# Performance work log

Measured on AMD Instinct MI355X. Metric: run time of the kernel, lower is better.

Reference implementation:

```python
import jax, jax.numpy as jnp
import numpy as np

N_AUTHOR, N_PAPER = 20000, 40000
E = 400000
IN_DIM, HIDDEN, HEADS, NUM_CLASSES, NUM_LAYERS = 128, 128, 8, 16, 2
DIM = HIDDEN // HEADS
NEG_SLOPE = 0.2
AUTHOR_RAW = 64


def setup_inputs() -> dict:
    key = jax.random.key(0)
    ks = jax.random.split(key, 16)
    s = 0.05
    return {
        'x_author': jax.random.normal(ks[0], (N_AUTHOR, AUTHOR_RAW), jnp.float32),
        'x_paper': jax.random.normal(ks[1], (N_PAPER, IN_DIM), jnp.float32),
        'Wa': jax.random.normal(ks[2], (AUTHOR_RAW, IN_DIM), jnp.float32) * s,
        'proj_w': jax.random.normal(ks[3], (NUM_LAYERS, 2, IN_DIM, HIDDEN), jnp.float32) * s,
        'proj_b': jnp.zeros((NUM_LAYERS, 2, HIDDEN), jnp.float32),
        'att_src': jax.random.normal(ks[4], (NUM_LAYERS, 3, HEADS, DIM), jnp.float32) * s,
        'att_dst': jax.random.normal(ks[5], (NUM_LAYERS, 3, HEADS, DIM), jnp.float32) * s,
        'klin_w': jax.random.normal(ks[6], (NUM_LAYERS, HIDDEN, HIDDEN), jnp.float32) * s,
        'klin_b': jnp.zeros((NUM_LAYERS, HIDDEN), jnp.float32),
        'q': jax.random.normal(ks[7], (NUM_LAYERS, HIDDEN), jnp.float32) * s,
        'lin_w': jax.random.normal(ks[8], (HIDDEN, NUM_CLASSES), jnp.float32) * s,
        'lin_b': jnp.zeros((NUM_CLASSES,), jnp.float32),
        'ei_writes': jnp.stack([jax.random.randint(ks[9], (E,), 0, N_AUTHOR),
                                jax.random.randint(ks[10], (E,), 0, N_PAPER)]),
        'ei_written_by': jnp.stack([jax.random.randint(ks[11], (E,), 0, N_PAPER),
                                    jax.random.randint(ks[12], (E,), 0, N_AUTHOR)]),
        'ei_cites': jnp.stack([jax.random.randint(ks[13], (E,), 0, N_PAPER),
                               jax.random.randint(ks[14], (E,), 0, N_PAPER)]),
    }


def _segment_softmax(scores, seg, num_segments):
    # scores: [E, H]; softmax over edges sharing a destination node.
    m = jax.ops.segment_max(scores, seg, num_segments=num_segments)
    m = jnp.where(jnp.isfinite(m), m, 0.0)
    e = jnp.exp(scores - m[seg])
    denom = jax.ops.segment_sum(e, seg, num_segments=num_segments)
    return e / (denom[seg] + 1e-16)


def _han_forward(x_author, x_paper, Wa, proj_w, proj_b, att_src, att_dst,
                 klin_w, klin_b, q, lin_w, lin_b,
                 ei_writes, ei_written_by, ei_cites):
    # Type-alignment projector (author: 64 -> 128, no bias; paper: Identity)
    x = {'author': x_author @ Wa, 'paper': x_paper}
    nsize = {'author': N_AUTHOR, 'paper': N_PAPER}
    ntidx = {'author': 0, 'paper': 1}
    edge_types = [('author', 'paper', ei_writes),
                  ('paper', 'author', ei_written_by),
                  ('paper', 'paper', ei_cites)]
    for l in range(NUM_LAYERS):
        # Per-node-type projection -> [N, H, D]
        xh = {nt: (x[nt] @ proj_w[l, ntidx[nt]] + proj_b[l, ntidx[nt]]).reshape(-1, HEADS, DIM)
              for nt in x}
        outs = {'author': [], 'paper': []}
        for e_id, (src, dst, ei) in enumerate(edge_types):
            a_src = (xh[src] * att_src[l, e_id]).sum(-1)  # [N_src, H]
            a_dst = (xh[dst] * att_dst[l, e_id]).sum(-1)  # [N_dst, H]
            si, di = ei[0], ei[1]
            alpha = a_src[si] + a_dst[di]                 # [E, H]
            alpha = jnp.where(alpha >= 0, alpha, NEG_SLOPE * alpha)  # leaky_relu
            alpha = _segment_softmax(alpha, di, nsize[dst])
            # attention dropout omitted (eval mode)
            msg = (xh[src][si] * alpha[:, :, None]).reshape(-1, HIDDEN)  # [E, HIDDEN]
            agg = jax.ops.segment_sum(msg, di, num_segments=nsize[dst])
            outs[dst].append(jax.nn.relu(agg))
        # Semantic-level attention over metapath embeddings per node type
        newx = {}
        for nt, xs in outs.items():
            stk = jnp.stack(xs)  # [M, N, F]
            score = (q[l] * jnp.tanh(stk @ klin_w[l] + klin_b[l]).mean(axis=1)).sum(-1)  # [M]
            attn = jax.nn.softmax(score)
            newx[nt] = (attn[:, None, None] * stk).sum(0)
        x = newx
        if l < NUM_LAYERS - 1:
            x = {nt: jax.nn.relu(v) for nt, v in x.items()}
            # feature dropout omitted (eval mode)
    return x['paper'] @ lin_w + lin_b  # [N_PAPER, NUM_CLASSES]


def reference(x_author, x_paper, Wa, proj_w, proj_b, att_src, att_dst,
              klin_w, klin_b, q, lin_w, lin_b,
              ei_writes, ei_written_by, ei_cites):
    return _han_forward(x_author, x_paper, Wa, proj_w, proj_b, att_src, att_dst,
                        klin_w, klin_b, q, lin_w, lin_b,
                        ei_writes, ei_written_by, ei_cites)
```

## Files before the change

### kernel.cpp

```cpp
#include <hip/hip_runtime.h>
#include <hip/hip_bf16.h>

typedef __hip_bfloat16 bf16;
typedef __hip_bfloat162 bf162;

#define N_AUTHOR 20000
#define N_PAPER  40000
#define NEDGE    400000
#define HID      128
#define HEADS    8
#define DIMH     16
#define NCLS     16

typedef short short4v __attribute__((ext_vector_type(4)));
typedef short short8v __attribute__((ext_vector_type(8)));
typedef float f32x4   __attribute__((ext_vector_type(4)));

__device__ __forceinline__ bf162 mk2(float a, float b){
    bf162 r; r.x = __float2bfloat16(a); r.y = __float2bfloat16(b); return r;
}
__device__ __forceinline__ float b2f(short s){
    return __uint_as_float(((unsigned)(unsigned short)s) << 16);
}
__device__ __forceinline__ short f2bs(float v){
    unsigned u = __float_as_uint(v);
    unsigned r = (u + 0x7FFFu + ((u >> 16) & 1u)) >> 16;
    return (short)r;
}
__device__ __forceinline__ float fastrcp(float x){ return __builtin_amdgcn_rcpf(x); }

__device__ __forceinline__ float fast_tanh(float x){
    x = fminf(fmaxf(x, -15.f), 15.f);
    float e = __expf(2.f * x);
    return 1.f - 2.f * fastrcp(e + 1.f);
}

template<int KDIM, int EPI>
__device__ __forceinline__ void bgemm_body(
    const bf16* __restrict__ A, const bf16* __restrict__ Wt, const float* __restrict__ Bb,
    bf16* __restrict__ C, const float* __restrict__ qv, float* __restrict__ score,
    int M, int brow, float* red)
{
    const int tid  = threadIdx.x;
    const int lane = tid & 63;
    const int wv   = tid >> 6;
    const int lr   = lane & 15;
    const int quad = lane >> 4;
    const int row0 = brow * 64 + wv * 16;
    const int arow_i = row0 + lr;
    const bool rowok = arow_i < M;
    const bf16* arow = A + (long)arow_i * KDIM;

    short8v afrag[KDIM / 32];
    #pragma unroll
    for (int kc = 0; kc < KDIM / 32; kc++) {
        short8v f = {0,0,0,0,0,0,0,0};
        if (rowok) f = *(const short8v*)(arow + kc * 32 + quad * 8);
        afrag[kc] = f;
    }

    f32x4 acc[8];
    #pragma unroll
    for (int ct = 0; ct < 8; ct++) acc[ct] = (f32x4){0.f, 0.f, 0.f, 0.f};

    #pragma unroll
    for (int k0 = 0; k0 < KDIM / 32; k0 += 2) {
        short8v bf[2][8];
        #pragma unroll
        for (int u = 0; u < 2; u++)
            #pragma unroll
            for (int ct = 0; ct < 8; ct++)
                bf[u][ct] = *(const short8v*)(Wt + (long)(ct * 16 + lr) * KDIM + (k0 + u) * 32 + quad * 8);
        #pragma unroll
        for (int u = 0; u < 2; u++)
            #pragma unroll
            for (int ct = 0; ct < 8; ct++)
                acc[ct] = __builtin_amdgcn_mfma_f32_16x16x32_bf16(afrag[k0 + u], bf[u][ct], acc[ct], 0, 0, 0);
    }

    if (EPI == 0) {
        #pragma unroll
        for (int ct = 0; ct < 8; ct++) {
            float bc = Bb ? Bb[ct * 16 + lr] : 0.f;
            #pragma unroll
            for (int r = 0; r < 4; r++) {
                int orow = row0 + quad * 4 + r;
                if (orow < M)
                    C[(long)orow * HID + ct * 16 + lr] = __float2bfloat16(acc[ct][r] + bc);
            }
        }
    } else {
        float part = 0.f;
        #pragma unroll
        for (int ct = 0; ct < 8; ct++) {
            float bc = Bb ? Bb[ct * 16 + lr] : 0.f;
            float qc = qv[ct * 16 + lr];
            #pragma unroll
            for (int r = 0; r < 4; r++) {
                int orow = row0 + quad * 4 + r;
                if (orow < M) part += qc * fast_tanh(acc[ct][r] + bc);
            }
        }
        red[tid] = part;
        __syncthreads();
        for (int s = 128; s > 0; s >>= 1) {
            if (tid < s) red[tid] += red[tid + s];
            __syncthreads();
        }
        if (tid == 0) atomicAdd(score, red[0]);
    }
}

template<int KDIM, int EPI>
__global__ __launch_bounds__(256) void bgemm_pair_kernel(
    const bf16* __restrict__ A0, const bf16* __restrict__ Wt0, const float* __restrict__ Bb0,
    bf16* __restrict__ C0, float* __restrict__ score0, int M0, int NB0,
    const bf16* __restrict__ A1, const bf16* __restrict__ Wt1, const float* __restrict__ Bb1,
    bf16* __restrict__ C1, float* __restrict__ score1, int M1,
    const float* __restrict__ qv)
{
    __shared__ float red[256];
    const int bx = blockIdx.x;
    if (bx < NB0)
        bgemm_body<KDIM, EPI>(A0, Wt0, Bb0, C0, qv, score0, M0, bx, red);
    else
        bgemm_body<KDIM, EPI>(A1, Wt1, Bb1, C1, qv, score1, M1, bx - NB0, red);
}

#define R_WA  (128 * 64)
#define R_PW  (4 * 128 * 128)
#define R_KW  (2 * 128 * 128)
#define NXA (N_AUTHOR * 64)
#define NXP (N_PAPER * HID)
#define CONV_W_TOT (R_WA + R_PW + R_KW)
#define CONV_X_TOT ((NXA + NXP) / 4)
#define CONV_TOT   (CONV_W_TOT + CONV_X_TOT)

#define CNT_OFF1 N_PAPER
#define CNT_OFF2 (N_PAPER + N_AUTHOR)
#define NDEST    (2 * N_PAPER + N_AUTHOR)
#define NCOPY 8
#define CW    2
#define CIDX(c, d) (((c) * NDEST + (d)) * CW)
#define CNT_TOT (NCOPY * NDEST * CW)
#define E3 (3 * NEDGE)
#define HIST_T (E3 / 4)

__global__ __launch_bounds__(256) void conv_hist_kernel(
    const int* __restrict__ d0, const int* __restrict__ d1, const int* __restrict__ d2,
    int* __restrict__ cnt, unsigned short* __restrict__ rank, int HB,
    const float* __restrict__ Wa, const float* __restrict__ proj_w,
    const float* __restrict__ klin_w,
    const float* __restrict__ xa_f, const float* __restrict__ xp_f,
    bf16* __restrict__ wt_wa, bf16* __restrict__ wt_proj, bf16* __restrict__ wt_klin,
    bf16* __restrict__ xa, bf16* __restrict__ xp)
{
    int bx = blockIdx.x;
    if (bx < HB) {
        int c = bx & (NCOPY - 1);
        int* mycnt = cnt + c * NDEST * CW;
        int t = bx * 256 + threadIdx.x;
        if (t >= HIST_T) return;
        #pragma unroll
        for (int u = 0; u < 4; u++) {
            int i = t + u * HIST_T;
            int r;
            if (i < NEDGE)            r = atomicAdd(&mycnt[d0[i] * CW], 1);
            else if (i < 2*NEDGE)     r = atomicAdd(&mycnt[(CNT_OFF1 + d1[i - NEDGE]) * CW], 1);
            else                      r = atomicAdd(&mycnt[(CNT_OFF2 + d2[i - 2*NEDGE]) * CW], 1);
            rank[i] = (unsigned short)((c << 13) | r);
        }
        return;
    }
    int t = (bx - HB) * 256 + threadIdx.x;
    if (t < CONV_W_TOT) {
        int i = t;
        if (i < R_WA) {
            int n = i >> 6, k = i & 63;
            wt_wa[i] = __float2bfloat16(Wa[k * 128 + n]);
        } else if (i < R_WA + R_PW) {
            int j = i - R_WA;
            int m = j >> 14, r = j & 16383;
            int n = r >> 7, k = r & 127;
            wt_proj[j] = __float2bfloat16(proj_w[m * 16384 + k * 128 + n]);
        } else {
            int j = i - R_WA - R_PW;
            int m = j >> 14, r = j & 16383;
            int n = r >> 7, k = r & 127;
            wt_klin[j] = __float2bfloat16(klin_w[m * 16384 + k * 128 + n]);
        }
    } else if (t < CONV_TOT) {
        int i = (t - CONV_W_TOT) * 4;
        if (i < NXA) {
            float4 v = *(const float4*)(xa_f + i);
            xa[i]   = __float2bfloat16(v.x); xa[i+1] = __float2bfloat16(v.y);
            xa[i+2] = __float2bfloat16(v.z); xa[i+3] = __float2bfloat16(v.w);
        } else {
            int j = i - NXA;
            float4 v = *(const float4*)(xp_f + j);
            xp[j]   = __float2bfloat16(v.x); xp[j+1] = __float2bfloat16(v.y);
            xp[j+2] = __float2bfloat16(v.z); xp[j+3] = __float2bfloat16(v.w);
        }
    }
}

__device__ __forceinline__ int job_nd(int j){ return j == 1 ? N_AUTHOR : N_PAPER; }
__device__ __forceinline__ int job_off(int j){ return j == 0 ? 0 : (j == 1 ? CNT_OFF1 : CNT_OFF2); }

__global__ __launch_bounds__(256) void scan_a3_kernel(const int* __restrict__ cnt,
                                                      int* __restrict__ bsum)
{
    int j = blockIdx.y;
    int nd = job_nd(j), off = job_off(j);
    __shared__ int s[256];
    int tid = threadIdx.x;
    int i = blockIdx.x * 256 + tid;
    int v = 0;
    if (i < nd) {
        #pragma unroll
        for (int c = 0; c < NCOPY; c++) v += cnt[CIDX(c, off + i)];
    }
    s[tid] = v;
    __syncthreads();
    for (int st = 128; st > 0; st >>= 1) {
        if (tid < st) s[tid] += s[tid + st];
        __syncthreads();
    }
    if (tid == 0) bsum[j * 256 + blockIdx.x] = s[0];
}

__global__ __launch_bounds__(256) void scan_b3_kernel(int* __restrict__ bsum,
    int* __restrict__ roff0, int* __restrict__ roff1, int* __restrict__ roff2)
{
    int j = blockIdx.x;
    int nd = job_nd(j);
    int nb = (nd + 255) / 256;
    int* roff = j == 0 ? roff0 : (j == 1 ? roff1 : roff2);
    __shared__ int s[256];
    int tid = threadIdx.x;
    int v = (tid < nb) ? bsum[j * 256 + tid] : 0;
    s[tid] = v;
    __syncthreads();
    for (int off = 1; off < 256; off <<= 1) {
        int t = (tid >= off) ? s[tid - off] : 0;
        __syncthreads();
        s[tid] += t;
        __syncthreads();
    }
    if (tid < nb) bsum[j * 256 + tid] = s[tid] - v;
    if (tid == 255) roff[nd] = s[255];
}

__global__ __launch_bounds__(256) void scan_c3_kernel(int* __restrict__ cnt,
    const int* __restrict__ bsum,
    int* __restrict__ roff0, int* __restrict__ roff1, int* __restrict__ roff2)
{
    int j = blockIdx.y;
    int nd = job_nd(j), off = job_off(j);
    int* roff = j == 0 ? roff0 : (j == 1 ? roff1 : roff2);
    __shared__ int s[256];
    int tid = threadIdx.x;
    int i = blockIdx.x * 256 + tid;
    int cc[NCOPY];
    int v = 0;
    if (i < nd) {
        #pragma unroll
        for (int c = 0; c < NCOPY; c++) { cc[c] = cnt[CIDX(c, off + i)]; v += cc[c]; }
    }
    s[tid] = v;
    __syncthreads();
    for (int o = 1; o < 256; o <<= 1) {
        int t = (tid >= o) ? s[tid - o] : 0;
        __syncthreads();
        s[tid] += t;
        __syncthreads();
    }
    if (i < nd) {
        int base = bsum[j * 256 + blockIdx.x] + s[tid] - v;
        roff[i] = base;
        #pragma unroll
        for (int c = 0; c < NCOPY; c++) { cnt[CIDX(c, off + i)] = base; base += cc[c]; }
    }
}

__global__ __launch_bounds__(256) void fill_gemm_kernel(
    const bf16* __restrict__ A, const bf16* __restrict__ Wt, bf16* __restrict__ C,
    int M, int GAb,
    const int* __restrict__ s0, const int* __restrict__ d0,
    const int* __restrict__ s1, const int* __restrict__ d1,
    const int* __restrict__ s2, const int* __restrict__ d2,
    const int* __restrict__ cnt,
    const unsigned short* __restrict__ rank,
    unsigned short* __restrict__ c0, unsigned short* __restrict__ c1, unsigned short* __restrict__ c2)
{
    __shared__ float red[256];
    int bx = blockIdx.x;
    if (bx < GAb) {
        bgemm_body<64, 0>(A, Wt, nullptr, C, nullptr, nullptr, M, bx, red);
        return;
    }
    int t = (bx - GAb) * 256 + threadIdx.x;
    if (t >= HIST_T) return;
    #pragma unroll
    for (int u = 0; u < 4; u++) {
        int i = t + u * HIST_T;
        int rw = rank[i];
        int c = rw >> 13, rk = rw & 0x1FFF;
        if (i < NEDGE) {
            int d = d0[i];
            c0[cnt[CIDX(c, d)] + rk] = (unsigned short)s0[i];
        } else if (i < 2*NEDGE) {
            int e = i - NEDGE, d = d1[e];
            c1[cnt[CIDX(c, CNT_OFF1 + d)] + rk] = (unsigned short)s1[e];
        } else {
            int e = i - 2*NEDGE, d = d2[e];
            c2[cnt[CIDX(c, CNT_OFF2 + d)] + rk] = (unsigned short)s2[e];
        }
    }
}

__global__ void node_att_multi_kernel(const bf16* __restrict__ xh,
    const float* __restrict__ A0, const float* __restrict__ A1,
    const float* __restrict__ A2, const float* __restrict__ A3,
    float* __restrict__ O0, float* __restrict__ O1,
    float* __restrict__ O2, float* __restrict__ O3, int N)
{
    int i = blockIdx.x * blockDim.x + threadIdx.x;
    if (i >= N * HEADS) return;
    int n = i >> 3, h = i & 7;
    const bf16* row = xh + (long)n * HID + h * DIMH;
    float x[DIMH];
    #pragma unroll
    for (int d = 0; d < DIMH; d++) x[d] = __bfloat162float(row[d]);
    if (A0) { float s = 0.f;
        #pragma unroll
        for (int d = 0; d < DIMH; d++) s += x[d] * A0[h*DIMH + d];
        O0[i] = s; }
    if (A1) { float s = 0.f;
        #pragma unroll
        for (int d = 0; d < DIMH; d++) s += x[d] * A1[h*DIMH + d];
        O1[i] = s; }
    if (A2) { float s = 0.f;
        #pragma unroll
        for (int d = 0; d < DIMH; d++) s += x[d] * A2[h*DIMH + d];
        O2[i] = s; }
    if (A3) { float s = 0.f;
        #pragma unroll
        for (int d = 0; d < DIMH; d++) s += x[d] * A3[h*DIMH + d];
        O3[i] = s; }
}

__global__ __launch_bounds__(256) void paper_gather2_kernel(
    const int* __restrict__ roff0, const unsigned short* __restrict__ csrc0,
    const float* __restrict__ as0, const float* __restrict__ ad0,
    const bf16* __restrict__ xha,
    const int* __restrict__ roff2, const unsigned short* __restrict__ csrc2,
    const float* __restrict__ as2, const float* __restrict__ ad2,
    const bf16* __restrict__ xhp,
    bf16* __restrict__ out0, bf16* __restrict__ out2)
{
    int lane = threadIdx.x & 63;
    int li   = lane & 15;
    int sub  = lane >> 4;
    int w = blockIdx.x * 16 + (threadIdx.x >> 6) * 4 + sub;
    if (w >= N_PAPER) return;
    int h = li >> 1;

    int b0 = roff0[w], n0 = roff0[w + 1] - b0;
    int b2 = roff2[w], n2 = roff2[w + 1] - b2;
    float ad0v = ad0[(long)w * 8 + h];
    float ad2v = ad2[(long)w * 8 + h];
    float den0 = 0.f, den2 = 0.f;
    float acc0[8], acc2[8];
    #pragma unroll
    for (int j = 0; j < 8; j++) { acc0[j] = 0.f; acc2[j] = 0.f; }

    int nmax = n0 > n2 ? n0 : n2;
    int c0m = n0 > 0 ? n0 - 1 : 0;
    int c2m = n2 > 0 ? n2 - 1 : 0;
    for (int i = 0; i < nmax; i += 4) {
        int sA[4], sB[4];
        #pragma unroll
        for (int u = 0; u < 4; u++) {
            sA[u] = csrc0[b0 + min(i + u, c0m)];
            sB[u] = csrc2[b2 + min(i + u, c2m)];
        }
        float aA[4], aB[4];
        short8v xA[4], xB[4];
        #pragma unroll
        for (int u = 0; u < 4; u++) {
            aA[u] = as0[(long)sA[u] * 8 + h];
            xA[u] = *(const short8v*)(xha + (long)sA[u] * HID + li * 8);
            aB[u] = as2[(long)sB[u] * 8 + h];
            xB[u] = *(const short8v*)(xhp + (long)sB[u] * HID + li * 8);
        }
        #pragma unroll
        for (int u = 0; u < 4; u++) {
            float a = aA[u] + ad0v;
            a = a >= 0.f ? a : 0.2f * a;
            float wt = __expf(fminf(a, 60.f));
            wt = (i + u < n0) ? wt : 0.f;
            den0 += wt;
            #pragma unroll
            for (int j = 0; j < 8; j++)
                acc0[j] = fmaf(b2f(xA[u][j]), wt, acc0[j]);
            a = aB[u] + ad2v;
            a = a >= 0.f ? a : 0.2f * a;
            wt = __expf(fminf(a, 60.f));
            wt = (i + u < n2) ? wt : 0.f;
            den2 += wt;
            #pragma unroll
            for (int j = 0; j < 8; j++)
                acc2[j] = fmaf(b2f(xB[u][j]), wt, acc2[j]);
        }
    }
    float inv0 = fastrcp(den0 + 1e-16f);
    float inv2 = fastrcp(den2 + 1e-16f);
    short8v o0, o2;
    #pragma unroll
    for (int j = 0; j < 8; j++) {
        o0[j] = f2bs(fmaxf(acc0[j] * inv0, 0.f));
        o2[j] = f2bs(fmaxf(acc2[j] * inv2, 0.f));
    }
    *(short8v*)(out0 + (long)w * HID + li * 8) = o0;
    *(short8v*)(out2 + (long)w * HID + li * 8) = o2;
}

__global__ __launch_bounds__(256) void edge_gather_kernel(
    const int* __restrict__ roff, const unsigned short* __restrict__ csrc,
    const float* __restrict__ as_, const float* __restrict__ ad_,
    const bf16* __restrict__ xh, bf16* __restrict__ out, int Ndst)
{
    int lane = threadIdx.x & 63;
    int li   = lane & 15;
    int sub  = lane >> 4;
    int w = blockIdx.x * 16 + (threadIdx.x >> 6) * 4 + sub;
    if (w >= Ndst) return;
    int h = li >> 1;
    int beg = roff[w], n = roff[w + 1] - beg;
    float adv = ad_[(long)w * 8 + h];
    float den = 0.f;
    float acc[8];
    #pragma unroll
    for (int j = 0; j < 8; j++) acc[j] = 0.f;
    int cm = n > 0 ? n - 1 : 0;
    for (int i = 0; i < n; i += 4) {
        int s[4];
        #pragma unroll
        for (int u = 0; u < 4; u++) s[u] = csrc[beg + min(i + u, cm)];
        float av[4]; short8v xv[4];
        #pragma unroll
        for (int u = 0; u < 4; u++) {
            av[u] = as_[(long)s[u] * 8 + h];
            xv[u] = *(const short8v*)(xh + (long)s[u] * HID + li * 8);
        }
        #pragma unroll
        for (int u = 0; u < 4; u++) {
            float a = av[u] + adv;
            a = a >= 0.f ? a : 0.2f * a;
            float wt = __expf(fminf(a, 60.f));
            wt = (i + u < n) ? wt : 0.f;
            den += wt;
            #pragma unroll
            for (int j = 0; j < 8; j++)
                acc[j] = fmaf(b2f(xv[u][j]), wt, acc[j]);
        }
    }
    float inv = fastrcp(den + 1e-16f);
    short8v o;
    #pragma unroll
    for (int j = 0; j < 8; j++) o[j] = f2bs(fmaxf(acc[j] * inv, 0.f));
    *(short8v*)(out + (long)w * HID + li * 8) = o;
}

__global__ void combine_kernel(const bf16* __restrict__ a0, const bf16* __restrict__ a1,
                               const float* __restrict__ score, bf16* __restrict__ out, int n2)
{
    int i = blockIdx.x * blockDim.x + threadIdx.x;
    if (i >= n2) return;
    float s0 = score[0] * (1.f / N_PAPER);
    float s1 = score[1] * (1.f / N_PAPER);
    float m = fmaxf(s0, s1);
    float e0 = __expf(s0 - m), e1 = __expf(s1 - m);
    float inv = fastrcp(e0 + e1);
    float w0 = e0 * inv, w1 = e1 * inv;
    bf162 v0 = ((const bf162*)a0)[i];
    bf162 v1 = ((const bf162*)a1)[i];
    ((bf162*)out)[i] = mk2(w0 * __bfloat162float(v0.x) + w1 * __bfloat162float(v1.x),
                           w0 * __bfloat162float(v0.y) + w1 * __bfloat162float(v1.y));
}

__global__ __launch_bounds__(256) void final_lin_fused_kernel(
    const bf16* __restrict__ a0, const bf16* __restrict__ a1,
    const float* __restrict__ score,
    const float* __restrict__ W, const float* __restrict__ B, float* __restrict__ out)
{
    __shared__ float Ws[HID * NCLS];
    int tid = threadIdx.x;
    for (int i = tid; i < HID * NCLS; i += 256) Ws[i] = W[i];
    __syncthreads();
    float s0 = score[0] * (1.f / N_PAPER);
    float s1 = score[1] * (1.f / N_PAPER);
    float m = fmaxf(s0, s1);
    float e0 = __expf(s0 - m), e1 = __expf(s1 - m);
    float inv = 1.f / (e0 + e1);
    float w0 = e0 * inv, w1 = e1 * inv;
    int i = blockIdx.x * 256 + tid;
    if (i >= N_PAPER * NCLS) return;
    int n = i >> 4, c = i & 15;
    float acc = B[c];
    const bf16* x0 = a0 + (long)n * HID;
    const bf16* x1 = a1 + (long)n * HID;
    #pragma unroll 16
    for (int k = 0; k < HID; k++)
        acc = fmaf(fmaf(w0, __bfloat162float(x0[k]), w1 * __bfloat162float(x1[k])),
                   Ws[k * NCLS + c], acc);
    out[i] = acc;
}

extern "C" void kernel_launch(void* const* d_in, const int* in_sizes, int n_in,
                              void* d_out, int out_size, void* d_ws, size_t ws_size,
                              hipStream_t stream)
{
    const float* x_author = (const float*)d_in[0];
    const float* x_paper  = (const float*)d_in[1];
    const float* Wa       = (const float*)d_in[2];
    const float* proj_w   = (const float*)d_in[3];
    const float* proj_b   = (const float*)d_in[4];
    const float* att_src  = (const float*)d_in[5];
    const float* att_dst  = (const float*)d_in[6];
    const float* klin_w   = (const float*)d_in[7];
    const float* klin_b   = (const float*)d_in[8];
    const float* qv       = (const float*)d_in[9];
    const float* lin_w    = (const float*)d_in[10];
    const float* lin_b    = (const float*)d_in[11];
    const int*  ei_w      = (const int*)d_in[12];
    const int*  ei_wb     = (const int*)d_in[13];
    const int*  ei_c      = (const int*)d_in[14];
    float* out = (float*)d_out;
    (void)ws_size; (void)in_sizes; (void)n_in; (void)out_size;

    char* base = (char*)d_ws;
    size_t off = 0;
    auto alloc = [&](size_t bytes) {
        void* p = base + off;
        off = (off + bytes + 255) & ~(size_t)255;
        return p;
    };
    bf16*  xh_a  = (bf16*) alloc((size_t)N_AUTHOR * HID * 2);
    bf16*  xh_p  = (bf16*) alloc((size_t)N_PAPER  * HID * 2);
    bf16*  buf_a = (bf16*) alloc((size_t)N_AUTHOR * HID * 2);
    bf16*  buf_p = (bf16*) alloc((size_t)N_PAPER  * HID * 2);
    bf16*  agg_p1= (bf16*) alloc((size_t)N_PAPER  * HID * 2);
    bf16*  xa    = (bf16*) alloc((size_t)N_AUTHOR * 64  * 2);
    bf16*  xp    = (bf16*) alloc((size_t)N_PAPER  * HID * 2);
    bf16*  wt_wa   = (bf16*)alloc((size_t)R_WA * 2);
    bf16*  wt_proj = (bf16*)alloc((size_t)R_PW * 2);
    bf16*  wt_klin = (bf16*)alloc((size_t)R_KW * 2);
    float* a_e0s = (float*)alloc((size_t)N_AUTHOR * HEADS * 4);
    float* a_e0d = (float*)alloc((size_t)N_PAPER  * HEADS * 4);
    float* a_e1s = (float*)alloc((size_t)N_PAPER  * HEADS * 4);
    float* a_e1d = (float*)alloc((size_t)N_AUTHOR * HEADS * 4);
    float* a_e2s = (float*)alloc((size_t)N_PAPER  * HEADS * 4);
    float* a_e2d = (float*)alloc((size_t)N_PAPER  * HEADS * 4);
    float* score  = (float*)alloc(64);
    int* roff0 = (int*)alloc((size_t)(N_PAPER  + 1) * 4);
    int* roff1 = (int*)alloc((size_t)(N_AUTHOR + 1) * 4);
    int* roff2 = (int*)alloc((size_t)(N_PAPER  + 1) * 4);
    unsigned short* csrc0 = (unsigned short*)alloc((size_t)NEDGE * 2 + 64);
    unsigned short* csrc1 = (unsigned short*)alloc((size_t)NEDGE * 2 + 64);
    unsigned short* csrc2 = (unsigned short*)alloc((size_t)NEDGE * 2 + 64);
    int* cnt   = (int*)alloc((size_t)CNT_TOT * 4);
    unsigned short* rank = (unsigned short*)alloc((size_t)E3 * 2);
    int* bsum  = (int*)alloc(3 * 256 * 4);

    const int GA = (N_AUTHOR + 63) / 64;
    const int GP = (N_PAPER  + 63) / 64;
    const int NBMAX = (N_PAPER + 255) / 256;
    const int HB = (HIST_T + 255) / 256;
    const int CONVB = (CONV_TOT + 255) / 256;

    hipMemsetAsync(cnt, 0, (size_t)CNT_TOT * 4, stream);
    conv_hist_kernel<<<HB + CONVB, 256, 0, stream>>>(
        ei_w + NEDGE, ei_wb + NEDGE, ei_c + NEDGE, cnt, rank, HB,
        Wa, proj_w, klin_w, x_author, x_paper,
        wt_wa, wt_proj, wt_klin, xa, xp);
    scan_a3_kernel<<<dim3(NBMAX, 3), 256, 0, stream>>>(cnt, bsum);
    scan_b3_kernel<<<3, 256, 0, stream>>>(bsum, roff0, roff1, roff2);
    scan_c3_kernel<<<dim3(NBMAX, 3), 256, 0, stream>>>(cnt, bsum, roff0, roff1, roff2);
    fill_gemm_kernel<<<GA + HB, 256, 0, stream>>>(
        xa, wt_wa, buf_a, N_AUTHOR, GA,
        ei_w, ei_w + NEDGE, ei_wb, ei_wb + NEDGE, ei_c, ei_c + NEDGE,
        cnt, rank, csrc0, csrc1, csrc2);

    for (int l = 0; l < 2; l++) {
        const bool last = (l == 1);
        const bf16* cur_a = buf_a;
        const bf16* cur_p = (l == 0) ? xp : buf_p;
        const bf16* pw_a = wt_proj + (size_t)(l*2 + 0) * HID * HID;
        const bf16* pw_p = wt_proj + (size_t)(l*2 + 1) * HID * HID;
        const float* pb_a = proj_b + (size_t)(l*2 + 0) * HID;
        const float* pb_p = proj_b + (size_t)(l*2 + 1) * HID;

        bgemm_pair_kernel<128, 0><<<GA + GP, 256, 0, stream>>>(
            cur_a, pw_a, pb_a, xh_a, nullptr, N_AUTHOR, GA,
            cur_p, pw_p, pb_p, xh_p, nullptr, N_PAPER, nullptr);

        hipMemsetAsync(score, 0, 64, stream);

        const float* as0 = att_src + (size_t)(l*3 + 0) * HID;
        const float* ad0 = att_dst + (size_t)(l*3 + 0) * HID;
        const float* as1 = att_src + (size_t)(l*3 + 1) * HID;
        const float* ad1 = att_dst + (size_t)(l*3 + 1) * HID;
        const float* as2 = att_src + (size_t)(l*3 + 2) * HID;
        const float* ad2 = att_dst + (size_t)(l*3 + 2) * HID;

        node_att_multi_kernel<<<(N_AUTHOR*HEADS + 255)/256, 256, 0, stream>>>(
            xh_a, as0, last ? nullptr : ad1, nullptr, nullptr,
            a_e0s, a_e1d, nullptr, nullptr, N_AUTHOR);
        node_att_multi_kernel<<<(N_PAPER*HEADS + 255)/256, 256, 0, stream>>>(
            xh_p, ad0, last ? nullptr : as1, as2, ad2,
            a_e0d, a_e1s, a_e2s, a_e2d, N_PAPER);

        paper_gather2_kernel<<<(N_PAPER + 15)/16, 256, 0, stream>>>(
            roff0, csrc0, a_e0s, a_e0d, xh_a,
            roff2, csrc2, a_e2s, a_e2d, xh_p,
            buf_p, agg_p1);
        if (!last)
            edge_gather_kernel<<<(N_AUTHOR + 15)/16, 256, 0, stream>>>(
                roff1, csrc1, a_e1s, a_e1d, xh_p, buf_a, N_AUTHOR);

        const bf16* kw = wt_klin + (size_t)l * HID * HID;
        const float* kb = klin_b + (size_t)l * HID;
        const float* qq = qv     + (size_t)l * HID;
        bgemm_pair_kernel<128, 1><<<2 * GP, 256, 0, stream>>>(
            buf_p, kw, kb, (bf16*)nullptr, score + 0, N_PAPER, GP,
            agg_p1, kw, kb, (bf16*)nullptr, score + 1, N_PAPER, qq);

        if (!last)
            combine_kernel<<<(N_PAPER*HID/2 + 255)/256, 256, 0, stream>>>(
                buf_p, agg_p1, score, buf_p, N_PAPER*HID/2);
    }

    final_lin_fused_kernel<<<(N_PAPER*NCLS + 255)/256, 256, 0, stream>>>(
        buf_p, agg_p1, score, lin_w, lin_b, out);
}
```

Baseline: 446.6 us.

## Fuse and reschedule kernels across stages to cut launches and passes

Unrolls the two-layer loop and merges many small launches. The histogram now runs alongside the author and paper projection GEMMs. Edge fill is merged with the author GEMM and paper node-attention, the three scan kernels become two, and the paper and author gathers share one launch. The semantic-attention combine is folded into the next layer's GEMM A-load, which removes a full read-write pass over paper features. The costs are more complex heterogeneous kernels, a redundant block-sum scan in every scan block, and possible register pressure in the blended GEMM.

```diff
diff --git a/kernel.cpp b/kernel.cpp
--- a/kernel.cpp
+++ b/kernel.cpp
@@ -12,13 +12,9 @@
 #define DIMH     16
 #define NCLS     16
 
-typedef short short4v __attribute__((ext_vector_type(4)));
 typedef short short8v __attribute__((ext_vector_type(8)));
 typedef float f32x4   __attribute__((ext_vector_type(4)));
 
-__device__ __forceinline__ bf162 mk2(float a, float b){
-    bf162 r; r.x = __float2bfloat16(a); r.y = __float2bfloat16(b); return r;
-}
 __device__ __forceinline__ float b2f(short s){
     return __uint_as_float(((unsigned)(unsigned short)s) << 16);
 }
@@ -35,9 +31,10 @@
     return 1.f - 2.f * fastrcp(e + 1.f);
 }
 
-template<int KDIM, int EPI>
+template<int KDIM, int EPI, int BLEND>
 __device__ __forceinline__ void bgemm_body(
-    const bf16* __restrict__ A, const bf16* __restrict__ Wt, const float* __restrict__ Bb,
+    const bf16* __restrict__ A, const bf16* __restrict__ A2, float w0, float w1,
+    const bf16* __restrict__ Wt, const float* __restrict__ Bb,
     bf16* __restrict__ C, const float* __restrict__ qv, float* __restrict__ score,
     int M, int brow, float* red)
 {
@@ -49,13 +46,22 @@
     const int row0 = brow * 64 + wv * 16;
     const int arow_i = row0 + lr;
     const bool rowok = arow_i < M;
-    const bf16* arow = A + (long)arow_i * KDIM;
+    const bf16* arow  = A  + (long)arow_i * KDIM;
+    const bf16* arow2 = BLEND ? (A2 + (long)arow_i * KDIM) : nullptr;
 
     short8v afrag[KDIM / 32];
     #pragma unroll
     for (int kc = 0; kc < KDIM / 32; kc++) {
         short8v f = {0,0,0,0,0,0,0,0};
-        if (rowok) f = *(const short8v*)(arow + kc * 32 + quad * 8);
+        if (rowok) {
+            f = *(const short8v*)(arow + kc * 32 + quad * 8);
+            if (BLEND) {
+                short8v g = *(const short8v*)(arow2 + kc * 32 + quad * 8);
+                #pragma unroll
+                for (int j = 0; j < 8; j++)
+                    f[j] = f2bs(w0 * b2f(f[j]) + w1 * b2f(g[j]));
+            }
+        }
         afrag[kc] = f;
     }
 
@@ -111,20 +117,31 @@
     }
 }
 
-template<int KDIM, int EPI>
+template<int KDIM, int EPI, int B1>
 __global__ __launch_bounds__(256) void bgemm_pair_kernel(
     const bf16* __restrict__ A0, const bf16* __restrict__ Wt0, const float* __restrict__ Bb0,
     bf16* __restrict__ C0, float* __restrict__ score0, int M0, int NB0,
-    const bf16* __restrict__ A1, const bf16* __restrict__ Wt1, const float* __restrict__ Bb1,
+    const bf16* __restrict__ A1, const bf16* __restrict__ A1b, const float* __restrict__ scw,
+    const bf16* __restrict__ Wt1, const float* __restrict__ Bb1,
     bf16* __restrict__ C1, float* __restrict__ score1, int M1,
     const float* __restrict__ qv)
 {
     __shared__ float red[256];
     const int bx = blockIdx.x;
-    if (bx < NB0)
-        bgemm_body<KDIM, EPI>(A0, Wt0, Bb0, C0, qv, score0, M0, bx, red);
-    else
-        bgemm_body<KDIM, EPI>(A1, Wt1, Bb1, C1, qv, score1, M1, bx - NB0, red);
+    if (bx < NB0) {
+        bgemm_body<KDIM, EPI, 0>(A0, nullptr, 0.f, 0.f, Wt0, Bb0, C0, qv, score0, M0, bx, red);
+    } else {
+        float w0 = 0.f, w1 = 0.f;
+        if (B1) {
+            float s0 = scw[0] * (1.f / N_PAPER);
+            float s1 = scw[1] * (1.f / N_PAPER);
+            float m = fmaxf(s0, s1);
+            float e0 = __expf(s0 - m), e1 = __expf(s1 - m);
+            float inv = fastrcp(e0 + e1);
+            w0 = e0 * inv; w1 = e1 * inv;
+        }
+        bgemm_body<KDIM, EPI, B1>(A1, A1b, w0, w1, Wt1, Bb1, C1, qv, score1, M1, bx - NB0, red);
+    }
 }
 
 #define R_WA  (128 * 64)
@@ -146,33 +163,14 @@
 #define E3 (3 * NEDGE)
 #define HIST_T (E3 / 4)
 
-__global__ __launch_bounds__(256) void conv_hist_kernel(
-    const int* __restrict__ d0, const int* __restrict__ d1, const int* __restrict__ d2,
-    int* __restrict__ cnt, unsigned short* __restrict__ rank, int HB,
+__global__ __launch_bounds__(256) void conv_kernel(
     const float* __restrict__ Wa, const float* __restrict__ proj_w,
     const float* __restrict__ klin_w,
     const float* __restrict__ xa_f, const float* __restrict__ xp_f,
     bf16* __restrict__ wt_wa, bf16* __restrict__ wt_proj, bf16* __restrict__ wt_klin,
     bf16* __restrict__ xa, bf16* __restrict__ xp)
 {
-    int bx = blockIdx.x;
-    if (bx < HB) {
-        int c = bx & (NCOPY - 1);
-        int* mycnt = cnt + c * NDEST * CW;
-        int t = bx * 256 + threadIdx.x;
-        if (t >= HIST_T) return;
-        #pragma unroll
-        for (int u = 0; u < 4; u++) {
-            int i = t + u * HIST_T;
-            int r;
-            if (i < NEDGE)            r = atomicAdd(&mycnt[d0[i] * CW], 1);
-            else if (i < 2*NEDGE)     r = atomicAdd(&mycnt[(CNT_OFF1 + d1[i - NEDGE]) * CW], 1);
-            else                      r = atomicAdd(&mycnt[(CNT_OFF2 + d2[i - 2*NEDGE]) * CW], 1);
-            rank[i] = (unsigned short)((c << 13) | r);
-        }
-        return;
-    }
-    int t = (bx - HB) * 256 + threadIdx.x;
+    int t = blockIdx.x * 256 + threadIdx.x;
     if (t < CONV_W_TOT) {
         int i = t;
         if (i < R_WA) {
@@ -204,6 +202,42 @@
     }
 }
 
+__global__ __launch_bounds__(256) void hist_gemm_kernel(
+    const int* __restrict__ d0, const int* __restrict__ d1, const int* __restrict__ d2,
+    int* __restrict__ cnt, unsigned short* __restrict__ rank, int HB,
+    const bf16* __restrict__ xa, const bf16* __restrict__ wt_wa, bf16* __restrict__ buf_a, int GA64,
+    const bf16* __restrict__ xp, const bf16* __restrict__ pw_p, const float* __restrict__ pb_p,
+    bf16* __restrict__ xh_p)
+{
+    __shared__ float red[256];
+    int bx = blockIdx.x;
+    if (bx < HB) {
+        int c = bx & (NCOPY - 1);
+        int* mycnt = cnt + c * NDEST * CW;
+        int t = bx * 256 + threadIdx.x;
+        if (t >= HIST_T) return;
+        #pragma unroll
+        for (int u = 0; u < 4; u++) {
+            int i = t + u * HIST_T;
+            int r;
+            if (i < NEDGE)            r = atomicAdd(&mycnt[d0[i] * CW], 1);
+            else if (i < 2*NEDGE)     r = atomicAdd(&mycnt[(CNT_OFF1 + d1[i - NEDGE]) * CW], 1);
+            else                      r = atomicAdd(&mycnt[(CNT_OFF2 + d2[i - 2*NEDGE]) * CW], 1);
+            rank[i] = (unsigned short)((c << 13) | r);
+        }
+        return;
+    }
+    bx -= HB;
+    if (bx < GA64) {
+        bgemm_body<64, 0, 0>(xa, nullptr, 0.f, 0.f, wt_wa, nullptr, buf_a,
+                             nullptr, nullptr, N_AUTHOR, bx, red);
+        return;
+    }
+    bx -= GA64;
+    bgemm_body<128, 0, 0>(xp, nullptr, 0.f, 0.f, pw_p, pb_p, xh_p,
+                          nullptr, nullptr, N_PAPER, bx, red);
+}
+
 __device__ __forceinline__ int job_nd(int j){ return j == 1 ? N_AUTHOR : N_PAPER; }
 __device__ __forceinline__ int job_off(int j){ return j == 0 ? 0 : (j == 1 ? CNT_OFF1 : CNT_OFF2); }
 
@@ -229,38 +263,29 @@
     if (tid == 0) bsum[j * 256 + blockIdx.x] = s[0];
 }
 
-__global__ __launch_bounds__(256) void scan_b3_kernel(int* __restrict__ bsum,
-    int* __restrict__ roff0, int* __restrict__ roff1, int* __restrict__ roff2)
-{
-    int j = blockIdx.x;
-    int nd = job_nd(j);
-    int nb = (nd + 255) / 256;
-    int* roff = j == 0 ? roff0 : (j == 1 ? roff1 : roff2);
-    __shared__ int s[256];
-    int tid = threadIdx.x;
-    int v = (tid < nb) ? bsum[j * 256 + tid] : 0;
-    s[tid] = v;
-    __syncthreads();
-    for (int off = 1; off < 256; off <<= 1) {
-        int t = (tid >= off) ? s[tid - off] : 0;
-        __syncthreads();
-        s[tid] += t;
-        __syncthreads();
-    }
-    if (tid < nb) bsum[j * 256 + tid] = s[tid] - v;
-    if (tid == 255) roff[nd] = s[255];
-}
-
-__global__ __launch_bounds__(256) void scan_c3_kernel(int* __restrict__ cnt,
+__global__ __launch_bounds__(256) void scan_bc_kernel(int* __restrict__ cnt,
     const int* __restrict__ bsum,
     int* __restrict__ roff0, int* __restrict__ roff1, int* __restrict__ roff2)
 {
     int j = blockIdx.y;
     int nd = job_nd(j), off = job_off(j);
     int* roff = j == 0 ? roff0 : (j == 1 ? roff1 : roff2);
+    __shared__ int sb[256];
     __shared__ int s[256];
     int tid = threadIdx.x;
-    int i = blockIdx.x * 256 + tid;
+    int bx = blockIdx.x;
+    int nb = (nd + 255) / 256;
+    int bvt = (tid < nb) ? bsum[j * 256 + tid] : 0;
+    sb[tid] = bvt;
+    __syncthreads();
+    for (int o = 1; o < 256; o <<= 1) {
+        int t = (tid >= o) ? sb[tid - o] : 0;
+        __syncthreads();
+        sb[tid] += t;
+        __syncthreads();
+    }
+    int base0 = sb[bx] - bsum[j * 256 + bx];
+    int i = bx * 256 + tid;
     int cc[NCOPY];
     int v = 0;
     if (i < nd) {
@@ -276,54 +301,80 @@
         __syncthreads();
     }
     if (i < nd) {
-        int base = bsum[j * 256 + blockIdx.x] + s[tid] - v;
+        int base = base0 + s[tid] - v;
         roff[i] = base;
         #pragma unroll
         for (int c = 0; c < NCOPY; c++) { cnt[CIDX(c, off + i)] = base; base += cc[c]; }
     }
-}
-
-__global__ __launch_bounds__(256) void fill_gemm_kernel(
-    const bf16* __restrict__ A, const bf16* __restrict__ Wt, bf16* __restrict__ C,
-    int M, int GAb,
+    if (bx == 0 && tid == 0) roff[nd] = NEDGE;
+}
+
+__global__ __launch_bounds__(256) void fill_natt_kernel(
     const int* __restrict__ s0, const int* __restrict__ d0,
     const int* __restrict__ s1, const int* __restrict__ d1,
     const int* __restrict__ s2, const int* __restrict__ d2,
-    const int* __restrict__ cnt,
-    const unsigned short* __restrict__ rank,
-    unsigned short* __restrict__ c0, unsigned short* __restrict__ c1, unsigned short* __restrict__ c2)
+    const int* __restrict__ cnt, const unsigned short* __restrict__ rank,
+    unsigned short* __restrict__ c0, unsigned short* __restrict__ c1, unsigned short* __restrict__ c2,
+    int HB,
+    const bf16* __restrict__ A, const bf16* __restrict__ Wt, const float* __restrict__ Bb,
+    bf16* __restrict__ C, int GAb,
+    const bf16* __restrict__ xh_p,
+    const float* __restrict__ ad0v, const float* __restrict__ as1v,
+    const float* __restrict__ as2v, const float* __restrict__ ad2v,
+    float* __restrict__ o_e0d, float* __restrict__ o_e1s,
+    float* __restrict__ o_e2s, float* __restrict__ o_e2d)
 {
     __shared__ float red[256];
     int bx = blockIdx.x;
+    if (bx < HB) {
+        int t = bx * 256 + threadIdx.x;
+        if (t >= HIST_T) return;
+        #pragma unroll
+        for (int u = 0; u < 4; u++) {
+            int i = t + u * HIST_T;
+            int rw = rank[i];
+            int c = rw >> 13, rk = rw & 0x1FFF;
+            if (i < NEDGE) {
+                int d = d0[i];
+                c0[cnt[CIDX(c, d)] + rk] = (unsigned short)s0[i];
+            } else if (i < 2*NEDGE) {
+                int e = i - NEDGE, d = d1[e];
+                c1[cnt[CIDX(c, CNT_OFF1 + d)] + rk] = (unsigned short)s1[e];
+            } else {
+                int e = i - 2*NEDGE, d = d2[e];
+                c2[cnt[CIDX(c, CNT_OFF2 + d)] + rk] = (unsigned short)s2[e];
+            }
+        }
+        return;
+    }
+    bx -= HB;
     if (bx < GAb) {
-        bgemm_body<64, 0>(A, Wt, nullptr, C, nullptr, nullptr, M, bx, red);
+        bgemm_body<128, 0, 0>(A, nullptr, 0.f, 0.f, Wt, Bb, C,
+                              nullptr, nullptr, N_AUTHOR, bx, red);
         return;
     }
-    int t = (bx - GAb) * 256 + threadIdx.x;
-    if (t >= HIST_T) return;
-    #pragma unroll
-    for (int u = 0; u < 4; u++) {
-        int i = t + u * HIST_T;
-        int rw = rank[i];
-        int c = rw >> 13, rk = rw & 0x1FFF;
-        if (i < NEDGE) {
-            int d = d0[i];
-            c0[cnt[CIDX(c, d)] + rk] = (unsigned short)s0[i];
-        } else if (i < 2*NEDGE) {
-            int e = i - NEDGE, d = d1[e];
-            c1[cnt[CIDX(c, CNT_OFF1 + d)] + rk] = (unsigned short)s1[e];
-        } else {
-            int e = i - 2*NEDGE, d = d2[e];
-            c2[cnt[CIDX(c, CNT_OFF2 + d)] + rk] = (unsigned short)s2[e];
-        }
-    }
+    bx -= GAb;
+    int i = bx * 256 + threadIdx.x;
+    if (i >= N_PAPER * HEADS) return;
+    int n = i >> 3, h = i & 7;
+    const bf16* row = xh_p + (long)n * HID + h * DIMH;
+    float x[DIMH];
+    #pragma unroll
+    for (int d = 0; d < DIMH; d++) x[d] = __bfloat162float(row[d]);
+    float sA = 0.f, sB = 0.f, sC = 0.f, sD = 0.f;
+    #pragma unroll
+    for (int d = 0; d < DIMH; d++) {
+        sA += x[d] * ad0v[h*DIMH + d];
+        sB += x[d] * as1v[h*DIMH + d];
+        sC += x[d] * as2v[h*DIMH + d];
+        sD += x[d] * ad2v[h*DIMH + d];
+    }
+    o_e0d[i] = sA; o_e1s[i] = sB; o_e2s[i] = sC; o_e2d[i] = sD;
 }
 
 __global__ void node_att_multi_kernel(const bf16* __restrict__ xh,
     const float* __restrict__ A0, const float* __restrict__ A1,
-    const float* __restrict__ A2, const float* __restrict__ A3,
-    float* __restrict__ O0, float* __restrict__ O1,
-    float* __restrict__ O2, float* __restrict__ O3, int N)
+    float* __restrict__ O0, float* __restrict__ O1, int N)
 {
     int i = blockIdx.x * blockDim.x + threadIdx.x;
     if (i >= N * HEADS) return;
@@ -340,17 +391,44 @@
         #pragma unroll
         for (int d = 0; d < DIMH; d++) s += x[d] * A1[h*DIMH + d];
         O1[i] = s; }
-    if (A2) { float s = 0.f;
-        #pragma unroll
-        for (int d = 0; d < DIMH; d++) s += x[d] * A2[h*DIMH + d];
-        O2[i] = s; }
-    if (A3) { float s = 0.f;
-        #pragma unroll
-        for (int d = 0; d < DIMH; d++) s += x[d] * A3[h*DIMH + d];
-        O3[i] = s; }
-}
-
-__global__ __launch_bounds__(256) void paper_gather2_kernel(
+}
+
+__global__ __launch_bounds__(256) void natt_l1_kernel(
+    const bf16* __restrict__ xh_a, const float* __restrict__ as0, float* __restrict__ a_e0s, int AB,
+    const bf16* __restrict__ xh_p, const float* __restrict__ ad0,
+    const float* __restrict__ as2, const float* __restrict__ ad2,
+    float* __restrict__ a_e0d, float* __restrict__ a_e2s, float* __restrict__ a_e2d)
+{
+    int bx = blockIdx.x, tid = threadIdx.x;
+    if (bx < AB) {
+        int i = bx * 256 + tid;
+        if (i >= N_AUTHOR * HEADS) return;
+        int n = i >> 3, h = i & 7;
+        const bf16* row = xh_a + (long)n * HID + h * DIMH;
+        float s = 0.f;
+        #pragma unroll
+        for (int d = 0; d < DIMH; d++) s += __bfloat162float(row[d]) * as0[h*DIMH + d];
+        a_e0s[i] = s;
+        return;
+    }
+    int i = (bx - AB) * 256 + tid;
+    if (i >= N_PAPER * HEADS) return;
+    int n = i >> 3, h = i & 7;
+    const bf16* row = xh_p + (long)n * HID + h * DIMH;
+    float x[DIMH];
+    #pragma unroll
+    for (int d = 0; d < DIMH; d++) x[d] = __bfloat162float(row[d]);
+    float sA = 0.f, sC = 0.f, sD = 0.f;
+    #pragma unroll
+    for (int d = 0; d < DIMH; d++) {
+        sA += x[d] * ad0[h*DIMH + d];
+        sC += x[d] * as2[h*DIMH + d];
+        sD += x[d] * ad2[h*DIMH + d];
+    }
+    a_e0d[i] = sA; a_e2s[i] = sC; a_e2d[i] = sD;
+}
+
+__device__ __forceinline__ void paper_gather2_dev(int bid,
     const int* __restrict__ roff0, const unsigned short* __restrict__ csrc0,
     const float* __restrict__ as0, const float* __restrict__ ad0,
     const bf16* __restrict__ xha,
@@ -362,7 +440,7 @@
     int lane = threadIdx.x & 63;
     int li   = lane & 15;
     int sub  = lane >> 4;
-    int w = blockIdx.x * 16 + (threadIdx.x >> 6) * 4 + sub;
+    int w = bid * 16 + (threadIdx.x >> 6) * 4 + sub;
     if (w >= N_PAPER) return;
     int h = li >> 1;
 
@@ -426,7 +504,7 @@
     *(short8v*)(out2 + (long)w * HID + li * 8) = o2;
 }
 
-__global__ __launch_bounds__(256) void edge_gather_kernel(
+__device__ __forceinline__ void edge_gather_dev(int bid,
     const int* __restrict__ roff, const unsigned short* __restrict__ csrc,
     const float* __restrict__ as_, const float* __restrict__ ad_,
     const bf16* __restrict__ xh, bf16* __restrict__ out, int Ndst)
@@ -434,7 +512,7 @@
     int lane = threadIdx.x & 63;
     int li   = lane & 15;
     int sub  = lane >> 4;
-    int w = blockIdx.x * 16 + (threadIdx.x >> 6) * 4 + sub;
+    int w = bid * 16 + (threadIdx.x >> 6) * 4 + sub;
     if (w >= Ndst) return;
     int h = li >> 1;
     int beg = roff[w], n = roff[w + 1] - beg;
@@ -473,21 +551,24 @@
     *(short8v*)(out + (long)w * HID + li * 8) = o;
 }
 
-__global__ void combine_kernel(const bf16* __restrict__ a0, const bf16* __restrict__ a1,
-                               const float* __restrict__ score, bf16* __restrict__ out, int n2)
-{
-    int i = blockIdx.x * blockDim.x + threadIdx.x;
-    if (i >= n2) return;
-    float s0 = score[0] * (1.f / N_PAPER);
-    float s1 = score[1] * (1.f / N_PAPER);
-    float m = fmaxf(s0, s1);
-    float e0 = __expf(s0 - m), e1 = __expf(s1 - m);
-    float inv = fastrcp(e0 + e1);
-    float w0 = e0 * inv, w1 = e1 * inv;
-    bf162 v0 = ((const bf162*)a0)[i];
-    bf162 v1 = ((const bf162*)a1)[i];
-    ((bf162*)out)[i] = mk2(w0 * __bfloat162float(v0.x) + w1 * __bfloat162float(v1.x),
-                           w0 * __bfloat162float(v0.y) + w1 * __bfloat162float(v1.y));
+__global__ __launch_bounds__(256) void gather_fused_kernel(
+    const int* __restrict__ roff0, const unsigned short* __restrict__ csrc0,
+    const float* __restrict__ as0, const float* __restrict__ ad0,
+    const bf16* __restrict__ xha,
+    const int* __restrict__ roff2, const unsigned short* __restrict__ csrc2,
+    const float* __restrict__ as2, const float* __restrict__ ad2,
+    const bf16* __restrict__ xhp,
+    bf16* __restrict__ out0, bf16* __restrict__ out2, int PB,
+    const int* __restrict__ roff1, const unsigned short* __restrict__ csrc1,
+    const float* __restrict__ as1, const float* __restrict__ ad1,
+    bf16* __restrict__ out_a)
+{
+    int bx = blockIdx.x;
+    if (bx < PB)
+        paper_gather2_dev(bx, roff0, csrc0, as0, ad0, xha,
+                          roff2, csrc2, as2, ad2, xhp, out0, out2);
+    else
+        edge_gather_dev(bx - PB, roff1, csrc1, as1, ad1, xhp, out_a, N_AUTHOR);
 }
 
 __global__ __launch_bounds__(256) void final_lin_fused_kernel(
@@ -579,69 +660,75 @@
     const int NBMAX = (N_PAPER + 255) / 256;
     const int HB = (HIST_T + 255) / 256;
     const int CONVB = (CONV_TOT + 255) / 256;
+    const int NATTP = (N_PAPER * HEADS + 255) / 256;
+    const int NATTA = (N_AUTHOR * HEADS + 255) / 256;
+    const int PGB = (N_PAPER + 15) / 16;
+    const int AGB = (N_AUTHOR + 15) / 16;
 
     hipMemsetAsync(cnt, 0, (size_t)CNT_TOT * 4, stream);
-    conv_hist_kernel<<<HB + CONVB, 256, 0, stream>>>(
-        ei_w + NEDGE, ei_wb + NEDGE, ei_c + NEDGE, cnt, rank, HB,
+    hipMemsetAsync(score, 0, 64, stream);
+
+    conv_kernel<<<CONVB, 256, 0, stream>>>(
         Wa, proj_w, klin_w, x_author, x_paper,
         wt_wa, wt_proj, wt_klin, xa, xp);
+    hist_gemm_kernel<<<HB + GA + GP, 256, 0, stream>>>(
+        ei_w + NEDGE, ei_wb + NEDGE, ei_c + NEDGE, cnt, rank, HB,
+        xa, wt_wa, buf_a, GA,
+        xp, wt_proj + (size_t)1 * HID * HID, proj_b + (size_t)1 * HID, xh_p);
     scan_a3_kernel<<<dim3(NBMAX, 3), 256, 0, stream>>>(cnt, bsum);
-    scan_b3_kernel<<<3, 256, 0, stream>>>(bsum, roff0, roff1, roff2);
-    scan_c3_kernel<<<dim3(NBMAX, 3), 256, 0, stream>>>(cnt, bsum, roff0, roff1, roff2);
-    fill_gemm_kernel<<<GA + HB, 256, 0, stream>>>(
-        xa, wt_wa, buf_a, N_AUTHOR, GA,
+    scan_bc_kernel<<<dim3(NBMAX, 3), 256, 0, stream>>>(cnt, bsum, roff0, roff1, roff2);
+
+    const float* as0_0 = att_src + 0 * HID; const float* ad0_0 = att_dst + 0 * HID;
+    const float* as1_0 = att_src + 1 * HID; const float* ad1_0 = att_dst + 1 * HID;
+    const float* as2_0 = att_src + 2 * HID; const float* ad2_0 = att_dst + 2 * HID;
+
+    fill_natt_kernel<<<HB + GA + NATTP, 256, 0, stream>>>(
         ei_w, ei_w + NEDGE, ei_wb, ei_wb + NEDGE, ei_c, ei_c + NEDGE,
-        cnt, rank, csrc0, csrc1, csrc2);
-
-    for (int l = 0; l < 2; l++) {
-        const bool last = (l == 1);
-        const bf16* cur_a = buf_a;
-        const bf16* cur_p = (l == 0) ? xp : buf_p;
-        const bf16* pw_a = wt_proj + (size_t)(l*2 + 0) * HID * HID;
-        const bf16* pw_p = wt_proj + (size_t)(l*2 + 1) * HID * HID;
-        const float* pb_a = proj_b + (size_t)(l*2 + 0) * HID;
-        const float* pb_p = proj_b + (size_t)(l*2 + 1) * HID;
-
-        bgemm_pair_kernel<128, 0><<<GA + GP, 256, 0, stream>>>(
-            cur_a, pw_a, pb_a, xh_a, nullptr, N_AUTHOR, GA,
-            cur_p, pw_p, pb_p, xh_p, nullptr, N_PAPER, nullptr);
-
-        hipMemsetAsync(score, 0, 64, stream);
-
-        const float* as0 = att_src + (size_t)(l*3 + 0) * HID;
-        const float* ad0 = att_dst + (size_t)(l*3 + 0) * HID;
-        const float* as1 = att_src + (size_t)(l*3 + 1) * HID;
-        const float* ad1 = att_dst + (size_t)(l*3 + 1) * HID;
-        const float* as2 = att_src + (size_t)(l*3 + 2) * HID;
-        const float* ad2 = att_dst + (size_t)(l*3 + 2) * HID;
-
-        node_att_multi_kernel<<<(N_AUTHOR*HEADS + 255)/256, 256, 0, stream>>>(
-            xh_a, as0, last ? nullptr : ad1, nullptr, nullptr,
-            a_e0s, a_e1d, nullptr, nullptr, N_AUTHOR);
-        node_att_multi_kernel<<<(N_PAPER*HEADS + 255)/256, 256, 0, stream>>>(
-            xh_p, ad0, last ? nullptr : as1, as2, ad2,
-            a_e0d, a_e1s, a_e2s, a_e2d, N_PAPER);
-
-        paper_gather2_kernel<<<(N_PAPER + 15)/16, 256, 0, stream>>>(
-            roff0, csrc0, a_e0s, a_e0d, xh_a,
-            roff2, csrc2, a_e2s, a_e2d, xh_p,
-            buf_p, agg_p1);
-        if (!last)
-            edge_gather_kernel<<<(N_AUTHOR + 15)/16, 256, 0, stream>>>(
-                roff1, csrc1, a_e1s, a_e1d, xh_p, buf_a, N_AUTHOR);
-
-        const bf16* kw = wt_klin + (size_t)l * HID * HID;
-        const float* kb = klin_b + (size_t)l * HID;
-        const float* qq = qv     + (size_t)l * HID;
-        bgemm_pair_kernel<128, 1><<<2 * GP, 256, 0, stream>>>(
-            buf_p, kw, kb, (bf16*)nullptr, score + 0, N_PAPER, GP,
-            agg_p1, kw, kb, (bf16*)nullptr, score + 1, N_PAPER, qq);
-
-        if (!last)
-            combine_kernel<<<(N_PAPER*HID/2 + 255)/256, 256, 0, stream>>>(
-                buf_p, agg_p1, score, buf_p, N_PAPER*HID/2);
-    }
-
-    final_lin_fused_kernel<<<(N_PAPER*NCLS + 255)/256, 256, 0, stream>>>(
+        cnt, rank, csrc0, csrc1, csrc2, HB,
+        buf_a, wt_proj + (size_t)0 * HID * HID, proj_b + (size_t)0 * HID, xh_a, GA,
+        xh_p, ad0_0, as1_0, as2_0, ad2_0,
+        a_e0d, a_e1s, a_e2s, a_e2d);
+    node_att_multi_kernel<<<NATTA, 256, 0, stream>>>(
+        xh_a, as0_0, ad1_0, a_e0s, a_e1d, N_AUTHOR);
+
+    gather_fused_kernel<<<PGB + AGB, 256, 0, stream>>>(
+        roff0, csrc0, a_e0s, a_e0d, xh_a,
+        roff2, csrc2, a_e2s, a_e2d, xh_p,
+        buf_p, agg_p1, PGB,
+        roff1, csrc1, a_e1s, a_e1d, buf_a);
+
+    bgemm_pair_kernel<128, 1, 0><<<2 * GP, 256, 0, stream>>>(
+        buf_p, wt_klin, klin_b, (bf16*)nullptr, score + 0, N_PAPER, GP,
+        agg_p1, nullptr, nullptr, wt_klin, klin_b, (bf16*)nullptr, score + 1, N_PAPER,
+        qv);
+
+    bgemm_pair_kernel<128, 0, 1><<<GA + GP, 256, 0, stream>>>(
+        buf_a, wt_proj + (size_t)2 * HID * HID, proj_b + (size_t)2 * HID, xh_a,
+        nullptr, N_AUTHOR, GA,
+        buf_p, agg_p1, score,
+        wt_proj + (size_t)3 * HID * HID, proj_b + (size_t)3 * HID, xh_p,
+        nullptr, N_PAPER, nullptr);
+    hipMemsetAsync(score, 0, 64, stream);
+
+    const float* as0_1 = att_src + 3 * HID; const float* ad0_1 = att_dst + 3 * HID;
+    const float* as2_1 = att_src + 5 * HID; const float* ad2_1 = att_dst + 5 * HID;
+
+    natt_l1_kernel<<<NATTA + NATTP, 256, 0, stream>>>(
+        xh_a, as0_1, a_e0s, NATTA,
+        xh_p, ad0_1, as2_1, ad2_1, a_e0d, a_e2s, a_e2d);
+
+    gather_fused_kernel<<<PGB, 256, 0, stream>>>(
+        roff0, csrc0, a_e0s, a_e0d, xh_a,
+        roff2, csrc2, a_e2s, a_e2d, xh_p,
+        buf_p, agg_p1, PGB,
+        roff1, csrc1, a_e1s, a_e1d, nullptr);
+
+    bgemm_pair_kernel<128, 1, 0><<<2 * GP, 256, 0, stream>>>(
+        buf_p, wt_klin + (size_t)HID * HID, klin_b + HID, (bf16*)nullptr, score + 0, N_PAPER, GP,
+        agg_p1, nullptr, nullptr, wt_klin + (size_t)HID * HID, klin_b + HID,
+        (bf16*)nullptr, score + 1, N_PAPER,
+        qv + HID);
+
+    final_lin_fused_kernel<<<(N_PAPER * NCLS + 255) / 256, 256, 0, stream>>>(
         buf_p, agg_p1, score, lin_w, lin_b, out);
 }
```

After: 427.5 us. 1.04x faster.
